# Kernel optimization log

Measured on AMD Instinct MI355X. Metric: run time of the kernel, lower is better.

Reference implementation:

```python
import jax, jax.numpy as jnp
import numpy as np

N, K, D = 16384, 2048, 512

def setup_inputs() -> dict:
    key = jax.random.key(0)
    kx, kmu, kstd = jax.random.split(key, 3)
    x = jax.random.normal(kx, (N, D), dtype=jnp.float32)
    mu = jax.random.normal(kmu, (K, D), dtype=jnp.float32)
    std = jax.random.uniform(kstd, (K, D), dtype=jnp.float32)  # positive so log(sum(std)) is defined
    return {"x": x, "mu": mu, "std": std}

def reference(x, mu, std):
    x_sq = jnp.sum(x * x, axis=1)                      # [N]
    mu_sq = jnp.sum(mu * mu, axis=1)                   # [K]
    sqdist = x_sq[:, None] - 2.0 * (x @ mu.T) + mu_sq[None, :]  # [N, K]
    denom = 2.0 * jnp.sum(std * std, axis=1) + 1e-8    # [K]
    log_std_sum = jnp.log(jnp.sum(std, axis=1))        # [K]
    half_log_2pi = 0.5 * jnp.log(jnp.asarray(2.0 * np.pi, dtype=x.dtype))
    return -sqdist / denom[None, :] - log_std_sum[None, :] - half_log_2pi
```

## Files before the change

kernel.cpp:

```cpp
#include <hip/hip_runtime.h>
#include <hip/hip_bf16.h>
#include <stdint.h>

#define NN 16384
#define KK 2048
#define DD 512

typedef __bf16 bf16x8 __attribute__((ext_vector_type(8)));
typedef float f32x4 __attribute__((ext_vector_type(4)));
typedef unsigned short ushort_t;
typedef ushort_t us8 __attribute__((ext_vector_type(8)));

#define AS1(p) ((const __attribute__((address_space(1))) void*)(p))
#define AS3(p) ((__attribute__((address_space(3))) void*)(p))

__device__ inline ushort_t f2bf(float f) {
  uint32_t u = __float_as_uint(f);
  u += 0x7fffu + ((u >> 16) & 1u);
  return (ushort_t)(u >> 16);
}

__global__ __launch_bounds__(256) void prep_x(const float* __restrict__ x,
                                              ushort_t* __restrict__ xb,
                                              float* __restrict__ x_sq) {
  const int wave = threadIdx.x >> 6;
  const int lane = threadIdx.x & 63;
  const int row = blockIdx.x * 4 + wave;
  const float* xr = x + (size_t)row * DD + lane * 8;
  float4 v0 = *reinterpret_cast<const float4*>(xr);
  float4 v1 = *reinterpret_cast<const float4*>(xr + 4);
  float s = v0.x*v0.x + v0.y*v0.y + v0.z*v0.z + v0.w*v0.w
          + v1.x*v1.x + v1.y*v1.y + v1.z*v1.z + v1.w*v1.w;
  us8 o;
  o[0]=f2bf(v0.x); o[1]=f2bf(v0.y); o[2]=f2bf(v0.z); o[3]=f2bf(v0.w);
  o[4]=f2bf(v1.x); o[5]=f2bf(v1.y); o[6]=f2bf(v1.z); o[7]=f2bf(v1.w);
  *reinterpret_cast<us8*>(xb + (size_t)row * DD + lane * 8) = o;
  #pragma unroll
  for (int off = 32; off; off >>= 1) s += __shfl_xor(s, off, 64);
  if (lane == 0) x_sq[row] = s;
}

__global__ __launch_bounds__(256) void prep_mu(const float* __restrict__ mu,
                                               const float* __restrict__ sd,
                                               ushort_t* __restrict__ mub,
                                               float* __restrict__ inv_denom,
                                               float* __restrict__ beta) {
  const int wave = threadIdx.x >> 6;
  const int lane = threadIdx.x & 63;
  const int row = blockIdx.x * 4 + wave;
  const float* mr = mu + (size_t)row * DD + lane * 8;
  float4 v0 = *reinterpret_cast<const float4*>(mr);
  float4 v1 = *reinterpret_cast<const float4*>(mr + 4);
  float musq = v0.x*v0.x + v0.y*v0.y + v0.z*v0.z + v0.w*v0.w
             + v1.x*v1.x + v1.y*v1.y + v1.z*v1.z + v1.w*v1.w;
  us8 o;
  o[0]=f2bf(v0.x); o[1]=f2bf(v0.y); o[2]=f2bf(v0.z); o[3]=f2bf(v0.w);
  o[4]=f2bf(v1.x); o[5]=f2bf(v1.y); o[6]=f2bf(v1.z); o[7]=f2bf(v1.w);
  *reinterpret_cast<us8*>(mub + (size_t)row * DD + lane * 8) = o;

  const float* sr = sd + (size_t)row * DD + lane * 8;
  float4 s0 = *reinterpret_cast<const float4*>(sr);
  float4 s1 = *reinterpret_cast<const float4*>(sr + 4);
  float ssum = s0.x + s0.y + s0.z + s0.w + s1.x + s1.y + s1.z + s1.w;
  float ssq  = s0.x*s0.x + s0.y*s0.y + s0.z*s0.z + s0.w*s0.w
             + s1.x*s1.x + s1.y*s1.y + s1.z*s1.z + s1.w*s1.w;
  #pragma unroll
  for (int off = 32; off; off >>= 1) {
    musq += __shfl_xor(musq, off, 64);
    ssum += __shfl_xor(ssum, off, 64);
    ssq  += __shfl_xor(ssq,  off, 64);
  }
  if (lane == 0) {
    float idn = 1.0f / (2.0f * ssq + 1e-8f);
    inv_denom[row] = idn;
    beta[row] = musq * idn + logf(ssum) + 0.91893853320467274f;
  }
}

__global__ __launch_bounds__(256) void gemm_eval(const ushort_t* __restrict__ xb,
                                                 const ushort_t* __restrict__ mub,
                                                 const float* __restrict__ x_sq,
                                                 const float* __restrict__ inv_denom,
                                                 const float* __restrict__ beta,
                                                 float* __restrict__ out) {
  __shared__ __align__(16) ushort_t As[128 * 32];
  __shared__ __align__(16) ushort_t Bs[128 * 32];

  const int t = threadIdx.x;
  const int lane = t & 63;
  const int w = t >> 6;
  const int wrow = w >> 1;
  const int wcol = w & 1;

  const int bm = blockIdx.x >> 4;
  const int bn = blockIdx.x & 15;
  const int brow = bm * 128;
  const int bcol = bn * 128;

  f32x4 acc[4][4];
  #pragma unroll
  for (int m = 0; m < 4; ++m)
    #pragma unroll
    for (int c = 0; c < 4; ++c)
      acc[m][c] = (f32x4){0.f, 0.f, 0.f, 0.f};

  const int c0 = t;
  const int c1 = t + 256;

  const int rl = lane & 15;
  const int slot = lane >> 4;

  for (int kt = 0; kt < DD / 32; ++kt) {
    const int kb = kt * 32;
    {
      const ushort_t* g0 = xb + (size_t)(brow + (c0 >> 2)) * DD + kb + (c0 & 3) * 8;
      __builtin_amdgcn_global_load_lds(AS1(g0), AS3(As + c0 * 8), 16, 0, 0);
      const ushort_t* g1 = xb + (size_t)(brow + (c1 >> 2)) * DD + kb + (c1 & 3) * 8;
      __builtin_amdgcn_global_load_lds(AS1(g1), AS3(As + c1 * 8), 16, 0, 0);
      const ushort_t* h0 = mub + (size_t)(bcol + (c0 >> 2)) * DD + kb + (c0 & 3) * 8;
      __builtin_amdgcn_global_load_lds(AS1(h0), AS3(Bs + c0 * 8), 16, 0, 0);
      const ushort_t* h1 = mub + (size_t)(bcol + (c1 >> 2)) * DD + kb + (c1 & 3) * 8;
      __builtin_amdgcn_global_load_lds(AS1(h1), AS3(Bs + c1 * 8), 16, 0, 0);
    }
    __syncthreads();

    const bf16x8* A8 = reinterpret_cast<const bf16x8*>(As);
    const bf16x8* B8 = reinterpret_cast<const bf16x8*>(Bs);
    bf16x8 af[4], bfr[4];
    #pragma unroll
    for (int m = 0; m < 4; ++m)
      af[m] = A8[(wrow * 64 + m * 16 + rl) * 4 + slot];
    #pragma unroll
    for (int c = 0; c < 4; ++c)
      bfr[c] = B8[(wcol * 64 + c * 16 + rl) * 4 + slot];

    #pragma unroll
    for (int m = 0; m < 4; ++m)
      #pragma unroll
      for (int c = 0; c < 4; ++c)
        acc[m][c] = __builtin_amdgcn_mfma_f32_16x16x32_bf16(af[m], bfr[c], acc[m][c], 0, 0, 0);

    __syncthreads();
  }

  const int rh = lane >> 4;
  float inv[4], bet[4];
  #pragma unroll
  for (int c = 0; c < 4; ++c) {
    int k = bcol + wcol * 64 + c * 16 + rl;
    inv[c] = inv_denom[k];
    bet[c] = beta[k];
  }
  #pragma unroll
  for (int m = 0; m < 4; ++m) {
    #pragma unroll
    for (int r = 0; r < 4; ++r) {
      int n = brow + wrow * 64 + m * 16 + rh * 4 + r;
      float xs = x_sq[n];
      size_t base = (size_t)n * KK + bcol + wcol * 64;
      #pragma unroll
      for (int c = 0; c < 4; ++c) {
        out[base + c * 16 + rl] = (2.0f * acc[m][c][r] - xs) * inv[c] - bet[c];
      }
    }
  }
}

extern "C" void kernel_launch(void* const* d_in, const int* in_sizes, int n_in,
                              void* d_out, int out_size, void* d_ws, size_t ws_size,
                              hipStream_t stream) {
  const float* x   = (const float*)d_in[0];
  const float* mu  = (const float*)d_in[1];
  const float* sd  = (const float*)d_in[2];
  float* out = (float*)d_out;

  char* ws = (char*)d_ws;
  ushort_t* xb        = (ushort_t*)(ws);
  ushort_t* mub       = (ushort_t*)(ws + 16777216);
  float*    x_sq      = (float*)(ws + 18874368);
  float*    inv_denom = (float*)(ws + 18939904);
  float*    beta      = (float*)(ws + 18948096);

  prep_x<<<NN / 4, 256, 0, stream>>>(x, xb, x_sq);
  prep_mu<<<KK / 4, 256, 0, stream>>>(mu, sd, mub, inv_denom, beta);
  gemm_eval<<<(NN / 128) * (KK / 128), 256, 0, stream>>>(xb, mub, x_sq, inv_denom, beta, out);
}
```

Measured before the change: 202.3 us.

## Pre-tile bf16 operands and triple-buffer the GEMM LDS pipeline

The prep kernels now write x and mu in a pre-tiled layout that matches the MFMA fragment order, so each K-tile is a contiguous 8 KB chunk and fragment reads from LDS are linear. The GEMM uses a three-stage LDS ring buffer, issuing async global-to-LDS loads two tiles ahead with explicit vmcnt waits and raw barriers. It also raises MFMA priority with setprio and swizzles block order for L2 locality. This is meant to hide global load latency behind the MFMAs and remove the full sync stall on every K step, at the cost of more LDS per block (48 KB) and fragile hand-written wait counts.

```diff
diff --git a/kernel.cpp b/kernel.cpp
--- a/kernel.cpp
+++ b/kernel.cpp
@@ -13,12 +13,15 @@
 
 #define AS1(p) ((const __attribute__((address_space(1))) void*)(p))
 #define AS3(p) ((__attribute__((address_space(3))) void*)(p))
+#define FENCE() asm volatile("" ::: "memory")
+#define SBAR()  do { FENCE(); __builtin_amdgcn_s_barrier(); FENCE(); } while (0)
 
 __device__ inline ushort_t f2bf(float f) {
   uint32_t u = __float_as_uint(f);
   u += 0x7fffu + ((u >> 16) & 1u);
   return (ushort_t)(u >> 16);
 }
+
 
 __global__ __launch_bounds__(256) void prep_x(const float* __restrict__ x,
                                               ushort_t* __restrict__ xb,
@@ -34,9 +37,14 @@
   us8 o;
   o[0]=f2bf(v0.x); o[1]=f2bf(v0.y); o[2]=f2bf(v0.z); o[3]=f2bf(v0.w);
   o[4]=f2bf(v1.x); o[5]=f2bf(v1.y); o[6]=f2bf(v1.z); o[7]=f2bf(v1.w);
-  *reinterpret_cast<us8*>(xb + (size_t)row * DD + lane * 8) = o;
-  #pragma unroll
-  for (int off = 32; off; off >>= 1) s += __shfl_xor(s, off, 64);
+
+  const int br = row >> 7, m = (row >> 4) & 7, r = row & 15;
+  const int kt = lane >> 2, slot = lane & 3;
+  size_t off = ((size_t)(br * 16 + kt)) * 4096 + m * 512 + slot * 128 + r * 8;
+  *reinterpret_cast<us8*>(xb + off) = o;
+
+  #pragma unroll
+  for (int offs = 32; offs; offs >>= 1) s += __shfl_xor(s, offs, 64);
   if (lane == 0) x_sq[row] = s;
 }
 
@@ -56,7 +64,11 @@
   us8 o;
   o[0]=f2bf(v0.x); o[1]=f2bf(v0.y); o[2]=f2bf(v0.z); o[3]=f2bf(v0.w);
   o[4]=f2bf(v1.x); o[5]=f2bf(v1.y); o[6]=f2bf(v1.z); o[7]=f2bf(v1.w);
-  *reinterpret_cast<us8*>(mub + (size_t)row * DD + lane * 8) = o;
+
+  const int bc = row >> 7, m = (row >> 4) & 7, r = row & 15;
+  const int kt = lane >> 2, slot = lane & 3;
+  size_t off = ((size_t)(bc * 16 + kt)) * 4096 + m * 512 + slot * 128 + r * 8;
+  *reinterpret_cast<us8*>(mub + off) = o;
 
   const float* sr = sd + (size_t)row * DD + lane * 8;
   float4 s0 = *reinterpret_cast<const float4*>(sr);
@@ -65,10 +77,10 @@
   float ssq  = s0.x*s0.x + s0.y*s0.y + s0.z*s0.z + s0.w*s0.w
              + s1.x*s1.x + s1.y*s1.y + s1.z*s1.z + s1.w*s1.w;
   #pragma unroll
-  for (int off = 32; off; off >>= 1) {
-    musq += __shfl_xor(musq, off, 64);
-    ssum += __shfl_xor(ssum, off, 64);
-    ssq  += __shfl_xor(ssq,  off, 64);
+  for (int offs = 32; offs; offs >>= 1) {
+    musq += __shfl_xor(musq, offs, 64);
+    ssum += __shfl_xor(ssum, offs, 64);
+    ssq  += __shfl_xor(ssq,  offs, 64);
   }
   if (lane == 0) {
     float idn = 1.0f / (2.0f * ssq + 1e-8f);
@@ -77,25 +89,26 @@
   }
 }
 
-__global__ __launch_bounds__(256) void gemm_eval(const ushort_t* __restrict__ xb,
-                                                 const ushort_t* __restrict__ mub,
-                                                 const float* __restrict__ x_sq,
-                                                 const float* __restrict__ inv_denom,
-                                                 const float* __restrict__ beta,
-                                                 float* __restrict__ out) {
-  __shared__ __align__(16) ushort_t As[128 * 32];
-  __shared__ __align__(16) ushort_t Bs[128 * 32];
-
-  const int t = threadIdx.x;
-  const int lane = t & 63;
-  const int w = t >> 6;
+__global__ __launch_bounds__(256, 3) void gemm_eval(const ushort_t* __restrict__ xb,
+                                                    const ushort_t* __restrict__ mub,
+                                                    const float* __restrict__ x_sq,
+                                                    const float* __restrict__ inv_denom,
+                                                    const float* __restrict__ beta,
+                                                    float* __restrict__ out) {
+  __shared__ __align__(16) ushort_t lds[3][8192];
+
+  const int t0 = threadIdx.x;
+  const int lane = t0 & 63;
+  const int w = t0 >> 6;
   const int wrow = w >> 1;
   const int wcol = w & 1;
 
-  const int bm = blockIdx.x >> 4;
-  const int bn = blockIdx.x & 15;
-  const int brow = bm * 128;
-  const int bcol = bn * 128;
+  const int bid = blockIdx.x;
+  const int swz = (bid & 7) * 256 + (bid >> 3);
+  const int bm = swz >> 4, bn = swz & 15;
+
+  const ushort_t* Aimg = xb  + (size_t)(bm * 16) * 4096;
+  const ushort_t* Bimg = mub + (size_t)(bn * 16) * 4096;
 
   f32x4 acc[4][4];
   #pragma unroll
@@ -104,64 +117,86 @@
     for (int c = 0; c < 4; ++c)
       acc[m][c] = (f32x4){0.f, 0.f, 0.f, 0.f};
 
-  const int c0 = t;
-  const int c1 = t + 256;
-
-  const int rl = lane & 15;
-  const int slot = lane >> 4;
-
-  for (int kt = 0; kt < DD / 32; ++kt) {
-    const int kb = kt * 32;
-    {
-      const ushort_t* g0 = xb + (size_t)(brow + (c0 >> 2)) * DD + kb + (c0 & 3) * 8;
-      __builtin_amdgcn_global_load_lds(AS1(g0), AS3(As + c0 * 8), 16, 0, 0);
-      const ushort_t* g1 = xb + (size_t)(brow + (c1 >> 2)) * DD + kb + (c1 & 3) * 8;
-      __builtin_amdgcn_global_load_lds(AS1(g1), AS3(As + c1 * 8), 16, 0, 0);
-      const ushort_t* h0 = mub + (size_t)(bcol + (c0 >> 2)) * DD + kb + (c0 & 3) * 8;
-      __builtin_amdgcn_global_load_lds(AS1(h0), AS3(Bs + c0 * 8), 16, 0, 0);
-      const ushort_t* h1 = mub + (size_t)(bcol + (c1 >> 2)) * DD + kb + (c1 & 3) * 8;
-      __builtin_amdgcn_global_load_lds(AS1(h1), AS3(Bs + c1 * 8), 16, 0, 0);
-    }
-    __syncthreads();
-
-    const bf16x8* A8 = reinterpret_cast<const bf16x8*>(As);
-    const bf16x8* B8 = reinterpret_cast<const bf16x8*>(Bs);
-    bf16x8 af[4], bfr[4];
+#define ISSUE(kt_) do {                                                                  \
+    const int b_ = (kt_) % 3;                                                            \
+    const ushort_t* a_ = Aimg + (size_t)(kt_) * 4096;                                    \
+    const ushort_t* bsrc_ = Bimg + (size_t)(kt_) * 4096;                                 \
+    __builtin_amdgcn_global_load_lds(AS1(a_ + t0 * 8),                                   \
+                                     AS3(&lds[b_][0] + t0 * 8), 16, 0, 0);               \
+    __builtin_amdgcn_global_load_lds(AS1(a_ + (t0 + 256) * 8),                           \
+                                     AS3(&lds[b_][0] + (t0 + 256) * 8), 16, 0, 0);       \
+    __builtin_amdgcn_global_load_lds(AS1(bsrc_ + t0 * 8),                                \
+                                     AS3(&lds[b_][4096] + t0 * 8), 16, 0, 0);            \
+    __builtin_amdgcn_global_load_lds(AS1(bsrc_ + (t0 + 256) * 8),                        \
+                                     AS3(&lds[b_][4096] + (t0 + 256) * 8), 16, 0, 0);    \
+  } while (0)
+
+#define TILE(t_, doIssue_, WAITASM) do {                                                 \
+    const ushort_t* Ab_ = &lds[(t_) % 3][0];                                             \
+    const ushort_t* Bb_ = &lds[(t_) % 3][4096];                                          \
+    bf16x8 af_[4], bf_[4];                                                               \
+    _Pragma("unroll") for (int m = 0; m < 4; ++m)                                        \
+      af_[m] = *reinterpret_cast<const bf16x8*>(Ab_ + (wrow * 4 + m) * 512 + lane * 8);  \
+    _Pragma("unroll") for (int c = 0; c < 4; ++c)                                        \
+      bf_[c] = *reinterpret_cast<const bf16x8*>(Bb_ + (wcol * 4 + c) * 512 + lane * 8);  \
+    if (doIssue_) ISSUE((t_) + 2);                                                       \
+    __builtin_amdgcn_s_setprio(1);                                                       \
+    _Pragma("unroll") for (int m = 0; m < 4; ++m)                                        \
+      _Pragma("unroll") for (int c = 0; c < 4; ++c)                                      \
+        acc[m][c] = __builtin_amdgcn_mfma_f32_16x16x32_bf16(af_[m], bf_[c],              \
+                                                            acc[m][c], 0, 0, 0);         \
+    __builtin_amdgcn_s_setprio(0);                                                       \
+    WAITASM;                                                                             \
+    SBAR();                                                                              \
+  } while (0)
+
+  ISSUE(0); ISSUE(1);
+  asm volatile("s_waitcnt vmcnt(4)" ::: "memory");
+  SBAR();
+
+  #pragma unroll
+  for (int t = 0; t < 14; ++t)
+    TILE(t, 1, asm volatile("s_waitcnt vmcnt(4)" ::: "memory"));
+  TILE(14, 0, asm volatile("s_waitcnt vmcnt(0)" ::: "memory"));
+  {
+    const ushort_t* Ab_ = &lds[15 % 3][0];
+    const ushort_t* Bb_ = &lds[15 % 3][4096];
+    bf16x8 af_[4], bf_[4];
     #pragma unroll
     for (int m = 0; m < 4; ++m)
-      af[m] = A8[(wrow * 64 + m * 16 + rl) * 4 + slot];
+      af_[m] = *reinterpret_cast<const bf16x8*>(Ab_ + (wrow * 4 + m) * 512 + lane * 8);
     #pragma unroll
     for (int c = 0; c < 4; ++c)
-      bfr[c] = B8[(wcol * 64 + c * 16 + rl) * 4 + slot];
-
+      bf_[c] = *reinterpret_cast<const bf16x8*>(Bb_ + (wcol * 4 + c) * 512 + lane * 8);
     #pragma unroll
     for (int m = 0; m < 4; ++m)
       #pragma unroll
       for (int c = 0; c < 4; ++c)
-        acc[m][c] = __builtin_amdgcn_mfma_f32_16x16x32_bf16(af[m], bfr[c], acc[m][c], 0, 0, 0);
-
-    __syncthreads();
-  }
-
-  const int rh = lane >> 4;
+        acc[m][c] = __builtin_amdgcn_mfma_f32_16x16x32_bf16(af_[m], bf_[c],
+                                                            acc[m][c], 0, 0, 0);
+  }
+#undef TILE
+#undef ISSUE
+
+  const int rl = lane & 15, rh = lane >> 4;
+  const int colbase = bn * 128 + wcol * 64;
   float inv[4], bet[4];
   #pragma unroll
   for (int c = 0; c < 4; ++c) {
-    int k = bcol + wcol * 64 + c * 16 + rl;
-    inv[c] = inv_denom[k];
-    bet[c] = beta[k];
+    inv[c] = inv_denom[colbase + c * 16 + rl];
+    bet[c] = beta[colbase + c * 16 + rl];
   }
   #pragma unroll
   for (int m = 0; m < 4; ++m) {
-    #pragma unroll
-    for (int r = 0; r < 4; ++r) {
-      int n = brow + wrow * 64 + m * 16 + rh * 4 + r;
-      float xs = x_sq[n];
-      size_t base = (size_t)n * KK + bcol + wcol * 64;
+    const int nb = bm * 128 + wrow * 64 + m * 16 + rh * 4;
+    #pragma unroll
+    for (int reg = 0; reg < 4; ++reg) {
+      const int n = nb + reg;
+      const float xs = x_sq[n];
+      float* op = out + (size_t)n * KK + colbase;
       #pragma unroll
-      for (int c = 0; c < 4; ++c) {
-        out[base + c * 16 + rl] = (2.0f * acc[m][c][r] - xs) * inv[c] - bet[c];
-      }
+      for (int c = 0; c < 4; ++c)
+        op[c * 16 + rl] = (2.0f * acc[m][c][reg] - xs) * inv[c] - bet[c];
     }
   }
 }
@@ -181,7 +216,7 @@
   float*    inv_denom = (float*)(ws + 18939904);
   float*    beta      = (float*)(ws + 18948096);
 
+  prep_mu<<<KK / 4, 256, 0, stream>>>(mu, sd, mub, inv_denom, beta);
   prep_x<<<NN / 4, 256, 0, stream>>>(x, xb, x_sq);
-  prep_mu<<<KK / 4, 256, 0, stream>>>(mu, sd, mub, inv_denom, beta);
   gemm_eval<<<(NN / 128) * (KK / 128), 256, 0, stream>>>(xb, mub, x_sq, inv_denom, beta, out);
 }
```

After: 192.1 us. -5.0%, faster.
